# Kernel optimization log

Measured on AMD Instinct MI355X. Metric: run time of the kernel, lower is better.

## Reference

```python
import jax, jax.numpy as jnp
import numpy as np

N, E = 50000, 800000
IN, HID, H1, H2, OUT = 128, 64, 4, 6, 121
NEG_SLOPE = 0.2


def setup_inputs() -> dict:
    key = jax.random.key(0)
    ks = jax.random.split(key, 16)
    s = 0.1  # weight init scale
    return {
        "x": jax.random.normal(ks[0], (N, IN), jnp.float32),
        "src": jax.random.randint(ks[1], (E,), 0, N),
        "dst": jax.random.randint(ks[2], (E,), 0, N),
        # conv1: in=IN, heads=H1, out=HID, concat
        "W1": jax.random.normal(ks[3], (IN, H1 * HID), jnp.float32) * s,
        "a1_src": jax.random.normal(ks[4], (H1, HID), jnp.float32) * s,
        "a1_dst": jax.random.normal(ks[5], (H1, HID), jnp.float32) * s,
        "b1": jnp.zeros((H1 * HID,), jnp.float32),
        # conv2: in=H1*HID, heads=H1, out=HID, concat, residual
        "W2": jax.random.normal(ks[6], (H1 * HID, H1 * HID), jnp.float32) * s,
        "a2_src": jax.random.normal(ks[7], (H1, HID), jnp.float32) * s,
        "a2_dst": jax.random.normal(ks[8], (H1, HID), jnp.float32) * s,
        "b2": jnp.zeros((H1 * HID,), jnp.float32),
        "Wres2": jax.random.normal(ks[9], (H1 * HID, H1 * HID), jnp.float32) * s,
        # conv3: in=H1*HID, heads=H2, out=OUT, mean (concat=False)
        "W3": jax.random.normal(ks[10], (H1 * HID, H2 * OUT), jnp.float32) * s,
        "a3_src": jax.random.normal(ks[11], (H2, OUT), jnp.float32) * s,
        "a3_dst": jax.random.normal(ks[12], (H2, OUT), jnp.float32) * s,
        "b3": jnp.zeros((OUT,), jnp.float32),
    }


def _segment_softmax(e, seg, n):
    # e: [E, H], softmax over edges sharing the same destination node
    m = jax.ops.segment_max(e, seg, num_segments=n)
    ex = jnp.exp(e - m[seg])
    s = jax.ops.segment_sum(ex, seg, num_segments=n)
    return ex / (s[seg] + 1e-16)


def _gat_conv(x, src, dst, W, a_src, a_dst, b, heads, ch, concat, Wres=None):
    n = x.shape[0]
    h = (x @ W).reshape(n, heads, ch)                       # [N, H, C]
    al_s = jnp.sum(h * a_src, axis=-1)                      # [N, H]
    al_d = jnp.sum(h * a_dst, axis=-1)                      # [N, H]
    e = jax.nn.leaky_relu(al_s[src] + al_d[dst], NEG_SLOPE)  # [E, H]
    alpha = _segment_softmax(e, dst, n)                     # [E, H]
    msg = h[src] * alpha[..., None]                         # [E, H, C]
    out = jax.ops.segment_sum(msg, dst, num_segments=n)     # [N, H, C]
    out = out.reshape(n, heads * ch) if concat else out.mean(axis=1)
    if Wres is not None:
        out = out + x @ Wres
    return out + b


def reference(x, src, dst, W1, a1_src, a1_dst, b1, W2, a2_src, a2_dst, b2,
              Wres2, W3, a3_src, a3_dst, b3):
    n = x.shape[0]
    # PyG GATConv default: add self-loops
    loop = jnp.arange(n, dtype=src.dtype)
    s = jnp.concatenate([src, loop])
    d = jnp.concatenate([dst, loop])
    h = jax.nn.elu(_gat_conv(x, s, d, W1, a1_src, a1_dst, b1, H1, HID, True))
    h = jax.nn.elu(_gat_conv(h, s, d, W2, a2_src, a2_dst, b2, H1, HID, True, Wres=Wres2))
    h = _gat_conv(h, s, d, W3, a3_src, a3_dst, b3, H2, OUT, False)
    return jax.nn.sigmoid(h)
```

## Files before the change

kernel.cpp:

```cpp
#include <hip/hip_runtime.h>
#include <hip/hip_bf16.h>


#define NODES 50000
#define EDGES 800000
#define MPAD  50048
#define C0    25088
#define C1    24912

typedef unsigned short u16;
typedef __attribute__((ext_vector_type(8))) short bf16x8;
typedef __attribute__((ext_vector_type(4))) float f32x4;

__device__ __forceinline__ float bf16f(u16 r) {
    return __uint_as_float(((unsigned)r) << 16);
}
__device__ __forceinline__ u16 f2b(float v) {
    __hip_bfloat16 b = __float2bfloat16(v);
    return *(u16*)&b;
}
__device__ __forceinline__ float blo(unsigned d) { return __uint_as_float(d << 16); }
__device__ __forceinline__ float bhi(unsigned d) { return __uint_as_float(d & 0xffff0000u); }


__global__ void fill_ones_kernel(int* __restrict__ deg, int n) {
    int i = blockIdx.x * blockDim.x + threadIdx.x;
    if (i < n) deg[i] = 1;
}

__global__ void hist_kernel(const int* __restrict__ dst, int* __restrict__ deg, int E) {
    int e = blockIdx.x * blockDim.x + threadIdx.x;
    if (e < E) atomicAdd(&deg[dst[e]], 1);
}

__global__ void deg_bsum_kernel(const int* __restrict__ deg, int* __restrict__ bsum, int n) {
    int tid = threadIdx.x, lane = tid & 63, wid = tid >> 6;
    int i = blockIdx.x * 256 + tid;
    int v = (i < n) ? deg[i] : 0;
    #pragma unroll
    for (int ofs = 32; ofs > 0; ofs >>= 1) v += __shfl_down(v, ofs);
    __shared__ int sp[4];
    if (lane == 0) sp[wid] = v;
    __syncthreads();
    if (tid == 0) bsum[blockIdx.x] = sp[0] + sp[1] + sp[2] + sp[3];
}

__global__ void bsum_scan_kernel(int* __restrict__ bsum, int* __restrict__ row_ptr,
                                 int nb, int n) {
    int tid = threadIdx.x, lane = tid & 63, wid = tid >> 6;
    int v = (tid < nb) ? bsum[tid] : 0;
    int incl = v;
    #pragma unroll
    for (int ofs = 1; ofs < 64; ofs <<= 1) {
        int t = __shfl_up(incl, ofs);
        if (lane >= ofs) incl += t;
    }
    __shared__ int sp[4];
    if (lane == 63) sp[wid] = incl;
    __syncthreads();
    int add = 0;
    for (int k = 0; k < wid; k++) add += sp[k];
    int excl = incl - v + add;
    if (tid < nb) bsum[tid] = excl;
    if (tid == nb - 1) row_ptr[n] = excl + v;
}

__global__ void deg_scan_kernel(const int* __restrict__ deg, const int* __restrict__ bofs,
                                int* __restrict__ row_ptr, int* __restrict__ cursor, int n) {
    int tid = threadIdx.x, lane = tid & 63, wid = tid >> 6;
    int i = blockIdx.x * 256 + tid;
    int v = (i < n) ? deg[i] : 0;
    int incl = v;
    #pragma unroll
    for (int ofs = 1; ofs < 64; ofs <<= 1) {
        int t = __shfl_up(incl, ofs);
        if (lane >= ofs) incl += t;
    }
    __shared__ int sp[4];
    if (lane == 63) sp[wid] = incl;
    __syncthreads();
    int add = bofs[blockIdx.x];
    for (int k = 0; k < wid; k++) add += sp[k];
    int excl = incl - v + add;
    if (i < n) { row_ptr[i] = excl; cursor[i] = excl; }
}

__global__ void scatter_kernel(const int* __restrict__ src, const int* __restrict__ dst,
                               int E, int n, int* __restrict__ cursor, int* __restrict__ csr_src) {
    int e = blockIdx.x * blockDim.x + threadIdx.x;
    if (e < E) {
        int d = dst[e];
        int p = atomicAdd(&cursor[d], 1);
        csr_src[p] = src[e];
    } else if (e < E + n) {
        int i = e - E;
        int p = atomicAdd(&cursor[i], 1);
        csr_src[p] = i;
    }
}


__global__ void convertA4_kernel(const float* __restrict__ A, u16* __restrict__ O, int total4) {
    int idx = blockIdx.x * blockDim.x + threadIdx.x;
    if (idx >= total4) return;
    float4 f = ((const float4*)A)[idx];
    ushort4 o;
    o.x = f2b(f.x); o.y = f2b(f.y); o.z = f2b(f.z); o.w = f2b(f.w);
    ((ushort4*)O)[idx] = o;
}

__global__ void convertW_kernel(const float* __restrict__ W, int ldw, int col0,
                                int Ncols, int Npad, int K, u16* __restrict__ WT) {
    int idx = blockIdx.x * blockDim.x + threadIdx.x;
    if (idx >= Npad * K) return;
    int k = idx % K;
    int n = idx / K;
    float f = (n < Ncols) ? W[(size_t)k * ldw + col0 + n] : 0.f;
    WT[(size_t)n * K + k] = f2b(f);
}

__global__ void convertW3stack_kernel(const float* __restrict__ W3, u16* __restrict__ WT) {
    int idx = blockIdx.x * blockDim.x + threadIdx.x;
    if (idx >= 128 * 1536) return;
    int q = idx % 1536;
    int n = idx / 1536;
    int h = q >> 8, k = q & 255;
    float f = (n < 121) ? W3[(size_t)k * 726 + h * 121 + n] : 0.f;
    WT[(size_t)n * 1536 + q] = f2b(f);
}

__global__ void prep_cmat_kernel(const float* __restrict__ W3, const float* __restrict__ a3s,
                                 const float* __restrict__ a3d, float* __restrict__ cm) {
    int idx = blockIdx.x * blockDim.x + threadIdx.x;
    if (idx >= 12 * 256) return;
    int k = idx & 255;
    int o = idx >> 8;
    int h = (o < 6) ? o : o - 6;
    const float* a = (o < 6) ? a3s : a3d;
    float v = 0.f;
    for (int c = 0; c < 121; c++) v += W3[(size_t)k * 726 + h * 121 + c] * a[h * 121 + c];
    cm[(size_t)o * 256 + k] = v;
}


__global__ __launch_bounds__(256) void gemm_mfma_kernel(
    const u16* __restrict__ A, const u16* __restrict__ B,
    u16* __restrict__ Cb, u16* __restrict__ Cb2,
    int M, int Ncols, int K2, int ldc, int split) {
    __shared__ __align__(16) u16 As[128][40];
    __shared__ __align__(16) u16 Bs[128][40];
    int tid = threadIdx.x;
    int lane = tid & 63;
    int wv = tid >> 6;
    int quad = lane >> 4, lm = lane & 15;
    int wm = (wv & 1) * 64, wn = (wv >> 1) * 64;
    int bm = blockIdx.x * 128, bn = blockIdx.y * 128;

    f32x4 zero = {0.f, 0.f, 0.f, 0.f};
    f32x4 acc[4][4];
    #pragma unroll
    for (int i = 0; i < 4; i++)
        #pragma unroll
        for (int j = 0; j < 4; j++) acc[i][j] = zero;

    for (int k0 = 0; k0 < K2; k0 += 32) {
        #pragma unroll
        for (int it = 0; it < 2; ++it) {
            int chunk = tid + it * 256;
            int row = chunk >> 2, seg = chunk & 3;
            uint4 va = *(const uint4*)(A + (size_t)(bm + row) * K2 + k0 + seg * 8);
            uint4 vb = *(const uint4*)(B + (size_t)(bn + row) * K2 + k0 + seg * 8);
            *(uint4*)&As[row][seg * 8] = va;
            *(uint4*)&Bs[row][seg * 8] = vb;
        }
        __syncthreads();
        bf16x8 af[4], bfr[4];
        #pragma unroll
        for (int i = 0; i < 4; i++) af[i] = *(const bf16x8*)&As[wm + i * 16 + lm][quad * 8];
        #pragma unroll
        for (int j = 0; j < 4; j++) bfr[j] = *(const bf16x8*)&Bs[wn + j * 16 + lm][quad * 8];
        #pragma unroll
        for (int i = 0; i < 4; i++)
            #pragma unroll
            for (int j = 0; j < 4; j++)
                acc[i][j] = __builtin_amdgcn_mfma_f32_16x16x32_bf16(af[i], bfr[j], acc[i][j], 0, 0, 0);
        __syncthreads();
    }

    #pragma unroll
    for (int i = 0; i < 4; i++) {
        #pragma unroll
        for (int j = 0; j < 4; j++) {
            int col = bn + wn + j * 16 + lm;
            if (col >= Ncols) continue;
            int row_base = bm + wm + i * 16 + quad * 4;
            #pragma unroll
            for (int r = 0; r < 4; r++) {
                int row = row_base + r;
                if (row >= M) continue;
                float v = acc[i][j][r];
                if (col < split) Cb[(size_t)row * ldc + col] = f2b(v);
                else             Cb2[(size_t)row * ldc + col - split] = f2b(v);
            }
        }
    }
}


__global__ __launch_bounds__(256) void gemm_skinny(
    const u16* __restrict__ A, const u16* __restrict__ B,
    float* __restrict__ C, const float* __restrict__ bias, int count) {
    __shared__ __align__(16) u16 Bs[128][40];
    int tid = threadIdx.x, lane = tid & 63, wv = tid >> 6;
    int quad = lane >> 4, lm = lane & 15;
    int bm = blockIdx.x * 32;
    int mrow = (wv >> 1) * 16;
    int ncol = (wv & 1) * 64;
    int arow = bm + mrow + lm;
    if (arow >= count) arow = count - 1;
    const u16* Ap = A + (size_t)arow * 1536;

    f32x4 zero = {0.f, 0.f, 0.f, 0.f};
    f32x4 acc[4];
    #pragma unroll
    for (int j = 0; j < 4; j++) acc[j] = zero;

    for (int k0 = 0; k0 < 1536; k0 += 32) {
        #pragma unroll
        for (int it = 0; it < 2; ++it) {
            int chunk = tid + it * 256;
            int r = chunk >> 2, s = chunk & 3;
            *(uint4*)&Bs[r][s * 8] = *(const uint4*)(B + (size_t)r * 1536 + k0 + s * 8);
        }
        bf16x8 af = *(const bf16x8*)(Ap + k0 + quad * 8);
        __syncthreads();
        #pragma unroll
        for (int j = 0; j < 4; j++) {
            bf16x8 bf = *(const bf16x8*)&Bs[ncol + j * 16 + lm][quad * 8];
            acc[j] = __builtin_amdgcn_mfma_f32_16x16x32_bf16(af, bf, acc[j], 0, 0, 0);
        }
        __syncthreads();
    }

    #pragma unroll
    for (int j = 0; j < 4; j++) {
        int col = ncol + j * 16 + lm;
        if (col >= 121) continue;
        int row_base = bm + mrow + quad * 4;
        #pragma unroll
        for (int r = 0; r < 4; r++) {
            int row = row_base + r;
            if (row >= count) continue;
            float v = acc[j][r] + bias[col];
            v = 1.f / (1.f + __expf(-v));
            C[(size_t)row * 121 + col] = v;
        }
    }
}


__global__ void row_alpha4_kernel(const u16* __restrict__ f, const float* __restrict__ a_s,
                                  const float* __restrict__ a_d, float* __restrict__ al_s,
                                  float* __restrict__ al_d, int n) {
    int wv = threadIdx.x >> 6, lane = threadIdx.x & 63;
    int i = blockIdx.x * 4 + wv;
    if (i >= n) return;
    ushort4 hv = *(const ushort4*)(f + (size_t)i * 256 + lane * 4);
    float4 as = *(const float4*)(a_s + lane * 4);
    float4 ad = *(const float4*)(a_d + lane * 4);
    float x0 = bf16f(hv.x), x1 = bf16f(hv.y), x2 = bf16f(hv.z), x3 = bf16f(hv.w);
    float ps = x0 * as.x + x1 * as.y + x2 * as.z + x3 * as.w;
    float pd = x0 * ad.x + x1 * ad.y + x2 * ad.z + x3 * ad.w;
    #pragma unroll
    for (int ofs = 1; ofs < 16; ofs <<= 1) {
        ps += __shfl_xor(ps, ofs);
        pd += __shfl_xor(pd, ofs);
    }
    if ((lane & 15) == 0) {
        int hd = lane >> 4;
        al_s[(size_t)i * 4 + hd] = ps;
        al_d[(size_t)i * 4 + hd] = pd;
    }
}

__global__ __launch_bounds__(256) void al3_kernel(const u16* __restrict__ o2b,
                                                  const float* __restrict__ cm,
                                                  float* __restrict__ al3, int n) {
    int wid = threadIdx.x >> 6, lane = threadIdx.x & 63;
    int i = blockIdx.x * 4 + wid;
    if (i >= n) return;
    uint2 d = *(const uint2*)(o2b + (size_t)i * 256 + lane * 4);
    float v0 = blo(d.x), v1 = bhi(d.x), v2 = blo(d.y), v3 = bhi(d.y);
    float a[12];
    #pragma unroll
    for (int o = 0; o < 12; o++) {
        float4 c = *(const float4*)(cm + (size_t)o * 256 + lane * 4);
        a[o] = v0 * c.x + v1 * c.y + v2 * c.z + v3 * c.w;
    }
    #pragma unroll
    for (int ofs = 1; ofs < 64; ofs <<= 1) {
        #pragma unroll
        for (int o = 0; o < 12; o++) a[o] += __shfl_xor(a[o], ofs);
    }
    if (lane == 0) {
        float4* dst = (float4*)(al3 + (size_t)i * 12);
        dst[0] = make_float4(a[0], a[1], a[2], a[3]);
        dst[1] = make_float4(a[4], a[5], a[6], a[7]);
        dst[2] = make_float4(a[8], a[9], a[10], a[11]);
    }
}


__global__ __launch_bounds__(256) void agg4_fused(
    const u16* __restrict__ f, const float* __restrict__ al_s, const float* __restrict__ al_d,
    const int* __restrict__ row_ptr, const int* __restrict__ csr_src,
    const float* __restrict__ bias, const u16* __restrict__ resb,
    u16* __restrict__ outb, int n) {
    int wid = threadIdx.x >> 6, lane = threadIdx.x & 63;
    int i = blockIdx.x * 4 + wid;
    if (i >= n) return;
    int beg = row_ptr[i], end = row_ptr[i + 1];
    int h_st = lane >> 4;
    int el = lane & 15;
    int half = lane >> 5;
    int c8 = (lane & 31) * 8;
    float ald_st = al_d[(size_t)i * 4 + h_st];
    float acc[8] = {};
    float S = 0.f;
    for (int base = beg; base < end; base += 16) {
        int cnt = min(16, end - base);
        int idxv = csr_src[base + min(el, cnt - 1)];
        float av = al_s[(size_t)idxv * 4 + h_st] + ald_st;
        av = av > 0.f ? av : 0.2f * av;
        float ex = __expf(fminf(av, 60.f));
        for (int e = 0; e < cnt; e += 2) {
            int ei = e + half;
            int eu = ei < cnt ? ei : e;
            int s = __shfl(idxv, eu);
            float w = __shfl(ex, ((lane & 24) << 1) | eu);
            if (ei >= cnt) w = 0.f;
            S += w;
            uint4 d = *(const uint4*)(f + (size_t)s * 256 + c8);
            acc[0] = fmaf(w, blo(d.x), acc[0]); acc[1] = fmaf(w, bhi(d.x), acc[1]);
            acc[2] = fmaf(w, blo(d.y), acc[2]); acc[3] = fmaf(w, bhi(d.y), acc[3]);
            acc[4] = fmaf(w, blo(d.z), acc[4]); acc[5] = fmaf(w, bhi(d.z), acc[5]);
            acc[6] = fmaf(w, blo(d.w), acc[6]); acc[7] = fmaf(w, bhi(d.w), acc[7]);
        }
    }
    #pragma unroll
    for (int k = 0; k < 8; k++) acc[k] += __shfl_xor(acc[k], 32);
    S += __shfl_xor(S, 32);
    if (half == 0) {
        float inv = 1.f / (S + 1e-16f);
        float4 b0 = *(const float4*)(bias + c8);
        float4 b1 = *(const float4*)(bias + c8 + 4);
        float v[8];
        v[0] = acc[0] * inv + b0.x; v[1] = acc[1] * inv + b0.y;
        v[2] = acc[2] * inv + b0.z; v[3] = acc[3] * inv + b0.w;
        v[4] = acc[4] * inv + b1.x; v[5] = acc[5] * inv + b1.y;
        v[6] = acc[6] * inv + b1.z; v[7] = acc[7] * inv + b1.w;
        if (resb) {
            uint4 r = *(const uint4*)(resb + (size_t)i * 256 + c8);
            v[0] += blo(r.x); v[1] += bhi(r.x); v[2] += blo(r.y); v[3] += bhi(r.y);
            v[4] += blo(r.z); v[5] += bhi(r.z); v[6] += blo(r.w); v[7] += bhi(r.w);
        }
        #pragma unroll
        for (int k = 0; k < 8; k++) v[k] = v[k] > 0.f ? v[k] : (__expf(v[k]) - 1.f);
        uint4 o;
        o.x = (unsigned)f2b(v[0]) | ((unsigned)f2b(v[1]) << 16);
        o.y = (unsigned)f2b(v[2]) | ((unsigned)f2b(v[3]) << 16);
        o.z = (unsigned)f2b(v[4]) | ((unsigned)f2b(v[5]) << 16);
        o.w = (unsigned)f2b(v[6]) | ((unsigned)f2b(v[7]) << 16);
        *(uint4*)(outb + (size_t)i * 256 + c8) = o;
    }
}


__global__ __launch_bounds__(256) void aggS_fused(
    const u16* __restrict__ x, const float* __restrict__ al3,
    const int* __restrict__ row_ptr, const int* __restrict__ csr_src,
    u16* __restrict__ S, int node0, int count) {
    __shared__ int s_i[4][16];
    __shared__ float s_w[4][96];
    int wid = threadIdx.x >> 6, lane = threadIdx.x & 63;
    int li = blockIdx.x * 4 + wid;
    if (li >= count) return;
    int i = node0 + li;
    int beg = row_ptr[i], end = row_ptr[i + 1];
    int half = lane >> 5;
    int c8 = (lane & 31) * 8;
    int e16 = lane & 15;
    int hA = lane >> 4;
    int hB = 4 + (lane >> 4);
    float aldA = al3[(size_t)i * 12 + 6 + hA];
    float aldB = (lane < 32) ? al3[(size_t)i * 12 + 6 + hB] : 0.f;
    float acc[6][8] = {};
    float Ssum[6] = {};
    for (int base = beg; base < end; base += 16) {
        int cnt = min(16, end - base);
        int idxe = csr_src[base + min(e16, cnt - 1)];
        if (lane < 16) s_i[wid][lane] = idxe;
        float vA = al3[(size_t)idxe * 12 + hA] + aldA;
        vA = vA > 0.f ? vA : 0.2f * vA;
        float exA = __expf(fminf(vA, 60.f));
        if (e16 < cnt) s_w[wid][e16 * 6 + hA] = exA;
        if (lane < 32) {
            float vB = al3[(size_t)idxe * 12 + hB] + aldB;
            vB = vB > 0.f ? vB : 0.2f * vB;
            float exB = __expf(fminf(vB, 60.f));
            if (e16 < cnt) s_w[wid][e16 * 6 + hB] = exB;
        }
        for (int e = 0; e < cnt; e += 2) {
            int ei = e + half;
            bool valid = ei < cnt;
            int eu = valid ? ei : e;
            int s = s_i[wid][eu];
            uint4 d = *(const uint4*)(x + (size_t)s * 256 + c8);
            float v0 = blo(d.x), v1 = bhi(d.x), v2 = blo(d.y), v3 = bhi(d.y);
            float v4 = blo(d.z), v5 = bhi(d.z), v6 = blo(d.w), v7 = bhi(d.w);
            #pragma unroll
            for (int hh = 0; hh < 6; hh++) {
                float w = valid ? s_w[wid][eu * 6 + hh] : 0.f;
                Ssum[hh] += w;
                acc[hh][0] = fmaf(w, v0, acc[hh][0]);
                acc[hh][1] = fmaf(w, v1, acc[hh][1]);
                acc[hh][2] = fmaf(w, v2, acc[hh][2]);
                acc[hh][3] = fmaf(w, v3, acc[hh][3]);
                acc[hh][4] = fmaf(w, v4, acc[hh][4]);
                acc[hh][5] = fmaf(w, v5, acc[hh][5]);
                acc[hh][6] = fmaf(w, v6, acc[hh][6]);
                acc[hh][7] = fmaf(w, v7, acc[hh][7]);
            }
        }
    }
    #pragma unroll
    for (int hh = 0; hh < 6; hh++) {
        Ssum[hh] += __shfl_xor(Ssum[hh], 32);
        #pragma unroll
        for (int k = 0; k < 8; k++) acc[hh][k] += __shfl_xor(acc[hh][k], 32);
    }
    if (half == 0) {
        #pragma unroll
        for (int hh = 0; hh < 6; hh++) {
            float inv = 1.f / (6.f * (Ssum[hh] + 1e-16f));
            uint4 o;
            o.x = (unsigned)f2b(acc[hh][0] * inv) | ((unsigned)f2b(acc[hh][1] * inv) << 16);
            o.y = (unsigned)f2b(acc[hh][2] * inv) | ((unsigned)f2b(acc[hh][3] * inv) << 16);
            o.z = (unsigned)f2b(acc[hh][4] * inv) | ((unsigned)f2b(acc[hh][5] * inv) << 16);
            o.w = (unsigned)f2b(acc[hh][6] * inv) | ((unsigned)f2b(acc[hh][7] * inv) << 16);
            *(uint4*)(S + (size_t)li * 1536 + hh * 256 + c8) = o;
        }
    }
}


extern "C" void kernel_launch(void* const* d_in, const int* in_sizes, int n_in,
                              void* d_out, int out_size, void* d_ws, size_t ws_size,
                              hipStream_t stream) {
    const float* x      = (const float*)d_in[0];
    const int*   src    = (const int*)d_in[1];
    const int*   dst    = (const int*)d_in[2];
    const float* W1     = (const float*)d_in[3];
    const float* a1_src = (const float*)d_in[4];
    const float* a1_dst = (const float*)d_in[5];
    const float* b1     = (const float*)d_in[6];
    const float* W2     = (const float*)d_in[7];
    const float* a2_src = (const float*)d_in[8];
    const float* a2_dst = (const float*)d_in[9];
    const float* b2     = (const float*)d_in[10];
    const float* Wres2  = (const float*)d_in[11];
    const float* W3     = (const float*)d_in[12];
    const float* a3_src = (const float*)d_in[13];
    const float* a3_dst = (const float*)d_in[14];
    const float* b3     = (const float*)d_in[15];
    float* out = (float*)d_out;

    const int N = NODES, E = EDGES;
    const int EN = E + N;
    const int NB = (N + 255) / 256;

    char* p = (char*)d_ws;
    auto alloc = [&](size_t bytes) -> char* {
        char* r = p;
        p += (bytes + 511) & ~(size_t)511;
        return r;
    };
    int*   row_ptr = (int*)alloc((size_t)(N + 1) * sizeof(int));
    int*   cursor  = (int*)alloc((size_t)N * sizeof(int));
    int*   deg     = (int*)alloc((size_t)N * sizeof(int));
    int*   bsum    = (int*)alloc(256 * sizeof(int));
    int*   csr_src = (int*)alloc((size_t)EN * sizeof(int));
    float* al      = (float*)alloc((size_t)N * 12 * sizeof(float));
    float* cm      = (float*)alloc((size_t)12 * 256 * sizeof(float));
    u16*   o2b     = (u16*)alloc((size_t)MPAD * 256 * sizeof(u16));
    u16*   WT2     = (u16*)alloc((size_t)512 * 256 * sizeof(u16));
    u16*   W3sT    = (u16*)alloc((size_t)128 * 1536 * sizeof(u16));
    const size_t A2B_B  = (size_t)MPAD * 256 * sizeof(u16);
    const size_t F1B_B  = (size_t)N * 256 * sizeof(u16);
    const size_t RESB_B = (size_t)N * 256 * sizeof(u16);
    const size_t S_B    = (size_t)C0 * 1536 * sizeof(u16);
    size_t r2_bytes = A2B_B + F1B_B + RESB_B;
    if (S_B > r2_bytes) r2_bytes = S_B;
    char* r2 = alloc(r2_bytes + 1024);
    u16* A2b  = (u16*)r2;
    u16* f1b  = (u16*)(r2 + A2B_B);
    u16* resb = (u16*)(r2 + A2B_B + F1B_B);
    u16* A2a  = (u16*)(r2 + A2B_B + F1B_B);
    u16* Sb   = (u16*)r2;
    (void)ws_size; (void)n_in; (void)in_sizes; (void)out_size;

    float* al_s = al;
    float* al_d = al + (size_t)4 * N;

    fill_ones_kernel<<<NB, 256, 0, stream>>>(deg, N);
    hist_kernel<<<(E + 255) / 256, 256, 0, stream>>>(dst, deg, E);
    deg_bsum_kernel<<<NB, 256, 0, stream>>>(deg, bsum, N);
    bsum_scan_kernel<<<1, 256, 0, stream>>>(bsum, row_ptr, NB, N);
    deg_scan_kernel<<<NB, 256, 0, stream>>>(deg, bsum, row_ptr, cursor, N);
    scatter_kernel<<<(E + N + 255) / 256, 256, 0, stream>>>(src, dst, E, N, cursor, csr_src);

    int nwb = (N + 3) / 4;

    convertA4_kernel<<<(N * 128 / 4 + 255) / 256, 256, 0, stream>>>(x, A2a, N * 128 / 4);
    convertW_kernel<<<(256 * 128 + 255) / 256, 256, 0, stream>>>(W1, 256, 0, 256, 256, 128, WT2);
    {
        dim3 g(MPAD / 128, 2);
        gemm_mfma_kernel<<<g, 256, 0, stream>>>(A2a, WT2, f1b, nullptr, N, 256, 128, 256, 9999);
    }
    row_alpha4_kernel<<<nwb, 256, 0, stream>>>(f1b, a1_src, a1_dst, al_s, al_d, N);
    agg4_fused<<<nwb, 256, 0, stream>>>(f1b, al_s, al_d, row_ptr, csr_src, b1, nullptr, A2b, N);

    convertW_kernel<<<(256 * 256 + 255) / 256, 256, 0, stream>>>(W2, 256, 0, 256, 256, 256, WT2);
    convertW_kernel<<<(256 * 256 + 255) / 256, 256, 0, stream>>>(Wres2, 256, 0, 256, 256, 256,
                                                                 WT2 + (size_t)256 * 256);
    {
        dim3 g(MPAD / 128, 4);
        gemm_mfma_kernel<<<g, 256, 0, stream>>>(A2b, WT2, f1b, resb, N, 512, 256, 256, 256);
    }
    row_alpha4_kernel<<<nwb, 256, 0, stream>>>(f1b, a2_src, a2_dst, al_s, al_d, N);
    agg4_fused<<<nwb, 256, 0, stream>>>(f1b, al_s, al_d, row_ptr, csr_src, b2, resb, o2b, N);

    prep_cmat_kernel<<<(12 * 256 + 255) / 256, 256, 0, stream>>>(W3, a3_src, a3_dst, cm);
    al3_kernel<<<nwb, 256, 0, stream>>>(o2b, cm, al, N);
    convertW3stack_kernel<<<(128 * 1536 + 255) / 256, 256, 0, stream>>>(W3, W3sT);
    {
        aggS_fused<<<(C0 + 3) / 4, 256, 0, stream>>>(o2b, al, row_ptr, csr_src, Sb, 0, C0);
        gemm_skinny<<<(C0 + 31) / 32, 256, 0, stream>>>(Sb, W3sT, out, b3, C0);
        aggS_fused<<<(C1 + 3) / 4, 256, 0, stream>>>(o2b, al, row_ptr, csr_src, Sb, C0, C1);
        gemm_skinny<<<(C1 + 31) / 32, 256, 0, stream>>>(Sb, W3sT, out + (size_t)C0 * 121, b3, C1);
    }
}
```

Measured before the change: 701.5 us.

## Fold attention-logit projections into weights and fuse prep and alpha kernels

Merges all weight conversions and the attention projection vectors (W·a) into one prep kernel. Layer-1 logits are computed from x during bf16 conversion, and later-layer logits are computed inside the previous aggregation epilogue. This removes the separate row_alpha/al3 passes and re-reads of the feature matrix. The final gemm now uses 64-row tiles with shared A staging, and aggS switches to 4 channels per lane without half-warp edge splitting. These trade extra epilogue FLOPs and different numerics (logits from fp32 instead of bf16 features) for fewer launches and memory passes.

```diff
diff --git a/kernel.cpp b/kernel.cpp
--- a/kernel.cpp
+++ b/kernel.cpp
@@ -100,46 +100,77 @@
 }
 
 
-__global__ void convertA4_kernel(const float* __restrict__ A, u16* __restrict__ O, int total4) {
-    int idx = blockIdx.x * blockDim.x + threadIdx.x;
-    if (idx >= total4) return;
-    float4 f = ((const float4*)A)[idx];
-    ushort4 o;
-    o.x = f2b(f.x); o.y = f2b(f.y); o.z = f2b(f.z); o.w = f2b(f.w);
-    ((ushort4*)O)[idx] = o;
-}
-
-__global__ void convertW_kernel(const float* __restrict__ W, int ldw, int col0,
-                                int Ncols, int Npad, int K, u16* __restrict__ WT) {
-    int idx = blockIdx.x * blockDim.x + threadIdx.x;
-    if (idx >= Npad * K) return;
-    int k = idx % K;
-    int n = idx / K;
-    float f = (n < Ncols) ? W[(size_t)k * ldw + col0 + n] : 0.f;
-    WT[(size_t)n * K + k] = f2b(f);
-}
-
-__global__ void convertW3stack_kernel(const float* __restrict__ W3, u16* __restrict__ WT) {
-    int idx = blockIdx.x * blockDim.x + threadIdx.x;
-    if (idx >= 128 * 1536) return;
-    int q = idx % 1536;
-    int n = idx / 1536;
-    int h = q >> 8, k = q & 255;
-    float f = (n < 121) ? W3[(size_t)k * 726 + h * 121 + n] : 0.f;
-    WT[(size_t)n * 1536 + q] = f2b(f);
-}
-
-__global__ void prep_cmat_kernel(const float* __restrict__ W3, const float* __restrict__ a3s,
-                                 const float* __restrict__ a3d, float* __restrict__ cm) {
-    int idx = blockIdx.x * blockDim.x + threadIdx.x;
-    if (idx >= 12 * 256) return;
-    int k = idx & 255;
-    int o = idx >> 8;
-    int h = (o < 6) ? o : o - 6;
-    const float* a = (o < 6) ? a3s : a3d;
-    float v = 0.f;
-    for (int c = 0; c < 121; c++) v += W3[(size_t)k * 726 + h * 121 + c] * a[h * 121 + c];
-    cm[(size_t)o * 256 + k] = v;
+__global__ void prep_weights(
+    const float* __restrict__ W1, const float* __restrict__ W2,
+    const float* __restrict__ Wres2, const float* __restrict__ W3,
+    const float* __restrict__ a1s, const float* __restrict__ a1d,
+    const float* __restrict__ a2s, const float* __restrict__ a2d,
+    const float* __restrict__ a3s, const float* __restrict__ a3d,
+    u16* __restrict__ WT1, u16* __restrict__ WT2, u16* __restrict__ W3sT,
+    float* __restrict__ q1t, float* __restrict__ q2t, float* __restrict__ cm) {
+    int idx = blockIdx.x * 256 + threadIdx.x;
+    if (idx < 32768) {
+        int n = idx >> 7, k = idx & 127;
+        WT1[idx] = f2b(W1[(size_t)k * 256 + n]);
+    } else if ((idx -= 32768) < 131072) {
+        int n = idx >> 8, k = idx & 255;
+        float v = (n < 256) ? W2[(size_t)k * 256 + n] : Wres2[(size_t)k * 256 + (n - 256)];
+        WT2[idx] = f2b(v);
+    } else if ((idx -= 131072) < 196608) {
+        int n = idx / 1536, q = idx % 1536;
+        int h = q >> 8, k = q & 255;
+        W3sT[idx] = f2b((n < 121) ? W3[(size_t)k * 726 + h * 121 + n] : 0.f);
+    } else if ((idx -= 196608) < 1024) {
+        int h = idx >> 7, k = idx & 127;
+        int hh = h & 3;
+        const float* a = (h < 4) ? a1s : a1d;
+        float v = 0.f;
+        for (int c = 0; c < 64; c++) v += W1[(size_t)k * 256 + hh * 64 + c] * a[hh * 64 + c];
+        q1t[idx] = v;
+    } else if ((idx -= 1024) < 2048) {
+        int h = idx >> 8, k = idx & 255;
+        int hh = h & 3;
+        const float* a = (h < 4) ? a2s : a2d;
+        float v = 0.f;
+        for (int c = 0; c < 64; c++) v += W2[(size_t)k * 256 + hh * 64 + c] * a[hh * 64 + c];
+        q2t[idx] = v;
+    } else if ((idx -= 2048) < 3072) {
+        int o = idx >> 8, k = idx & 255;
+        int h = (o < 6) ? o : o - 6;
+        const float* a = (o < 6) ? a3s : a3d;
+        float v = 0.f;
+        for (int c = 0; c < 121; c++) v += W3[(size_t)k * 726 + h * 121 + c] * a[h * 121 + c];
+        cm[idx] = v;
+    }
+}
+#define PREP_TOTAL (32768 + 131072 + 196608 + 1024 + 2048 + 3072)
+
+
+__global__ __launch_bounds__(256) void convx_al1(
+    const float* __restrict__ x, const float* __restrict__ q1t,
+    u16* __restrict__ A2a, float* __restrict__ alA, int n) {
+    int wid = threadIdx.x >> 6, lane = threadIdx.x & 63;
+    int i = blockIdx.x * 4 + wid;
+    if (i >= n) return;
+    float2 xv = *(const float2*)(x + (size_t)i * 128 + lane * 2);
+    ushort2 o;
+    o.x = f2b(xv.x); o.y = f2b(xv.y);
+    *(ushort2*)(A2a + (size_t)i * 128 + lane * 2) = o;
+    float p[8];
+    #pragma unroll
+    for (int h = 0; h < 8; h++) {
+        float2 q = *(const float2*)(q1t + h * 128 + lane * 2);
+        p[h] = xv.x * q.x + xv.y * q.y;
+    }
+    #pragma unroll
+    for (int ofs = 1; ofs <= 32; ofs <<= 1) {
+        #pragma unroll
+        for (int h = 0; h < 8; h++) p[h] += __shfl_xor(p[h], ofs);
+    }
+    if (lane == 0) {
+        *(float4*)(alA + (size_t)i * 8)     = make_float4(p[0], p[1], p[2], p[3]);
+        *(float4*)(alA + (size_t)i * 8 + 4) = make_float4(p[4], p[5], p[6], p[7]);
+    }
 }
 
 
@@ -207,115 +238,75 @@
 }
 
 
-__global__ __launch_bounds__(256) void gemm_skinny(
+__global__ __launch_bounds__(256) void gemm_skinny64(
     const u16* __restrict__ A, const u16* __restrict__ B,
     float* __restrict__ C, const float* __restrict__ bias, int count) {
+    __shared__ __align__(16) u16 As[64][40];
     __shared__ __align__(16) u16 Bs[128][40];
     int tid = threadIdx.x, lane = tid & 63, wv = tid >> 6;
     int quad = lane >> 4, lm = lane & 15;
-    int bm = blockIdx.x * 32;
-    int mrow = (wv >> 1) * 16;
-    int ncol = (wv & 1) * 64;
-    int arow = bm + mrow + lm;
-    if (arow >= count) arow = count - 1;
-    const u16* Ap = A + (size_t)arow * 1536;
+    int bm = blockIdx.x * 64;
+    int mrow = (wv >> 1) * 32, ncol = (wv & 1) * 64;
+    int ar = bm + (tid >> 2);
+    if (ar >= count) ar = count - 1;
+    const u16* Ap = A + (size_t)ar * 1536 + (tid & 3) * 8;
 
     f32x4 zero = {0.f, 0.f, 0.f, 0.f};
-    f32x4 acc[4];
-    #pragma unroll
-    for (int j = 0; j < 4; j++) acc[j] = zero;
+    f32x4 acc[2][4];
+    #pragma unroll
+    for (int i = 0; i < 2; i++)
+        #pragma unroll
+        for (int j = 0; j < 4; j++) acc[i][j] = zero;
 
     for (int k0 = 0; k0 < 1536; k0 += 32) {
+        *(uint4*)&As[tid >> 2][(tid & 3) * 8] = *(const uint4*)(Ap + k0);
         #pragma unroll
         for (int it = 0; it < 2; ++it) {
-            int chunk = tid + it * 256;
-            int r = chunk >> 2, s = chunk & 3;
-            *(uint4*)&Bs[r][s * 8] = *(const uint4*)(B + (size_t)r * 1536 + k0 + s * 8);
-        }
-        bf16x8 af = *(const bf16x8*)(Ap + k0 + quad * 8);
+            int t = tid + it * 256;
+            *(uint4*)&Bs[t >> 2][(t & 3) * 8] =
+                *(const uint4*)(B + (size_t)(t >> 2) * 1536 + k0 + (t & 3) * 8);
+        }
         __syncthreads();
+        bf16x8 af[2], bfr[4];
+        #pragma unroll
+        for (int i = 0; i < 2; i++) af[i] = *(const bf16x8*)&As[mrow + i * 16 + lm][quad * 8];
+        #pragma unroll
+        for (int j = 0; j < 4; j++) bfr[j] = *(const bf16x8*)&Bs[ncol + j * 16 + lm][quad * 8];
+        #pragma unroll
+        for (int i = 0; i < 2; i++)
+            #pragma unroll
+            for (int j = 0; j < 4; j++)
+                acc[i][j] = __builtin_amdgcn_mfma_f32_16x16x32_bf16(af[i], bfr[j], acc[i][j], 0, 0, 0);
+        __syncthreads();
+    }
+
+    #pragma unroll
+    for (int i = 0; i < 2; i++) {
         #pragma unroll
         for (int j = 0; j < 4; j++) {
-            bf16x8 bf = *(const bf16x8*)&Bs[ncol + j * 16 + lm][quad * 8];
-            acc[j] = __builtin_amdgcn_mfma_f32_16x16x32_bf16(af, bf, acc[j], 0, 0, 0);
-        }
-        __syncthreads();
-    }
-
-    #pragma unroll
-    for (int j = 0; j < 4; j++) {
-        int col = ncol + j * 16 + lm;
-        if (col >= 121) continue;
-        int row_base = bm + mrow + quad * 4;
-        #pragma unroll
-        for (int r = 0; r < 4; r++) {
-            int row = row_base + r;
-            if (row >= count) continue;
-            float v = acc[j][r] + bias[col];
-            v = 1.f / (1.f + __expf(-v));
-            C[(size_t)row * 121 + col] = v;
-        }
-    }
-}
-
-
-__global__ void row_alpha4_kernel(const u16* __restrict__ f, const float* __restrict__ a_s,
-                                  const float* __restrict__ a_d, float* __restrict__ al_s,
-                                  float* __restrict__ al_d, int n) {
-    int wv = threadIdx.x >> 6, lane = threadIdx.x & 63;
-    int i = blockIdx.x * 4 + wv;
-    if (i >= n) return;
-    ushort4 hv = *(const ushort4*)(f + (size_t)i * 256 + lane * 4);
-    float4 as = *(const float4*)(a_s + lane * 4);
-    float4 ad = *(const float4*)(a_d + lane * 4);
-    float x0 = bf16f(hv.x), x1 = bf16f(hv.y), x2 = bf16f(hv.z), x3 = bf16f(hv.w);
-    float ps = x0 * as.x + x1 * as.y + x2 * as.z + x3 * as.w;
-    float pd = x0 * ad.x + x1 * ad.y + x2 * ad.z + x3 * ad.w;
-    #pragma unroll
-    for (int ofs = 1; ofs < 16; ofs <<= 1) {
-        ps += __shfl_xor(ps, ofs);
-        pd += __shfl_xor(pd, ofs);
-    }
-    if ((lane & 15) == 0) {
-        int hd = lane >> 4;
-        al_s[(size_t)i * 4 + hd] = ps;
-        al_d[(size_t)i * 4 + hd] = pd;
-    }
-}
-
-__global__ __launch_bounds__(256) void al3_kernel(const u16* __restrict__ o2b,
-                                                  const float* __restrict__ cm,
-                                                  float* __restrict__ al3, int n) {
-    int wid = threadIdx.x >> 6, lane = threadIdx.x & 63;
-    int i = blockIdx.x * 4 + wid;
-    if (i >= n) return;
-    uint2 d = *(const uint2*)(o2b + (size_t)i * 256 + lane * 4);
-    float v0 = blo(d.x), v1 = bhi(d.x), v2 = blo(d.y), v3 = bhi(d.y);
-    float a[12];
-    #pragma unroll
-    for (int o = 0; o < 12; o++) {
-        float4 c = *(const float4*)(cm + (size_t)o * 256 + lane * 4);
-        a[o] = v0 * c.x + v1 * c.y + v2 * c.z + v3 * c.w;
-    }
-    #pragma unroll
-    for (int ofs = 1; ofs < 64; ofs <<= 1) {
-        #pragma unroll
-        for (int o = 0; o < 12; o++) a[o] += __shfl_xor(a[o], ofs);
-    }
-    if (lane == 0) {
-        float4* dst = (float4*)(al3 + (size_t)i * 12);
-        dst[0] = make_float4(a[0], a[1], a[2], a[3]);
-        dst[1] = make_float4(a[4], a[5], a[6], a[7]);
-        dst[2] = make_float4(a[8], a[9], a[10], a[11]);
+            int col = ncol + j * 16 + lm;
+            if (col >= 121) continue;
+            int row_base = bm + mrow + i * 16 + quad * 4;
+            #pragma unroll
+            for (int r = 0; r < 4; r++) {
+                int row = row_base + r;
+                if (row >= count) continue;
+                float v = acc[i][j][r] + bias[col];
+                v = 1.f / (1.f + __expf(-v));
+                C[(size_t)row * 121 + col] = v;
+            }
+        }
     }
 }
 
 
 __global__ __launch_bounds__(256) void agg4_fused(
-    const u16* __restrict__ f, const float* __restrict__ al_s, const float* __restrict__ al_d,
+    const u16* __restrict__ f, const float* __restrict__ al8,
     const int* __restrict__ row_ptr, const int* __restrict__ csr_src,
     const float* __restrict__ bias, const u16* __restrict__ resb,
-    u16* __restrict__ outb, int n) {
+    u16* __restrict__ outb,
+    const float* __restrict__ q8, float* __restrict__ alB,
+    const float* __restrict__ q12, float* __restrict__ al12, int n) {
     int wid = threadIdx.x >> 6, lane = threadIdx.x & 63;
     int i = blockIdx.x * 4 + wid;
     if (i >= n) return;
@@ -324,13 +315,13 @@
     int el = lane & 15;
     int half = lane >> 5;
     int c8 = (lane & 31) * 8;
-    float ald_st = al_d[(size_t)i * 4 + h_st];
+    float ald_st = al8[(size_t)i * 8 + 4 + h_st];
     float acc[8] = {};
     float S = 0.f;
     for (int base = beg; base < end; base += 16) {
         int cnt = min(16, end - base);
         int idxv = csr_src[base + min(el, cnt - 1)];
-        float av = al_s[(size_t)idxv * 4 + h_st] + ald_st;
+        float av = al8[(size_t)idxv * 8 + h_st] + ald_st;
         av = av > 0.f ? av : 0.2f * av;
         float ex = __expf(fminf(av, 60.f));
         for (int e = 0; e < cnt; e += 2) {
@@ -372,6 +363,47 @@
         o.z = (unsigned)f2b(v[4]) | ((unsigned)f2b(v[5]) << 16);
         o.w = (unsigned)f2b(v[6]) | ((unsigned)f2b(v[7]) << 16);
         *(uint4*)(outb + (size_t)i * 256 + c8) = o;
+        if (alB) {
+            float pj[8];
+            #pragma unroll
+            for (int h = 0; h < 8; h++) {
+                const float* qp = q8 + h * 256 + c8;
+                float4 qa = *(const float4*)qp;
+                float4 qb = *(const float4*)(qp + 4);
+                pj[h] = v[0] * qa.x + v[1] * qa.y + v[2] * qa.z + v[3] * qa.w
+                      + v[4] * qb.x + v[5] * qb.y + v[6] * qb.z + v[7] * qb.w;
+            }
+            #pragma unroll
+            for (int ofs = 1; ofs <= 16; ofs <<= 1) {
+                #pragma unroll
+                for (int h = 0; h < 8; h++) pj[h] += __shfl_xor(pj[h], ofs);
+            }
+            if (lane == 0) {
+                *(float4*)(alB + (size_t)i * 8)     = make_float4(pj[0], pj[1], pj[2], pj[3]);
+                *(float4*)(alB + (size_t)i * 8 + 4) = make_float4(pj[4], pj[5], pj[6], pj[7]);
+            }
+        }
+        if (al12) {
+            float pj[12];
+            #pragma unroll
+            for (int o12 = 0; o12 < 12; o12++) {
+                const float* qp = q12 + o12 * 256 + c8;
+                float4 qa = *(const float4*)qp;
+                float4 qb = *(const float4*)(qp + 4);
+                pj[o12] = v[0] * qa.x + v[1] * qa.y + v[2] * qa.z + v[3] * qa.w
+                        + v[4] * qb.x + v[5] * qb.y + v[6] * qb.z + v[7] * qb.w;
+            }
+            #pragma unroll
+            for (int ofs = 1; ofs <= 16; ofs <<= 1) {
+                #pragma unroll
+                for (int o12 = 0; o12 < 12; o12++) pj[o12] += __shfl_xor(pj[o12], ofs);
+            }
+            if (lane == 0) {
+                *(float4*)(al12 + (size_t)i * 12)     = make_float4(pj[0], pj[1], pj[2], pj[3]);
+                *(float4*)(al12 + (size_t)i * 12 + 4) = make_float4(pj[4], pj[5], pj[6], pj[7]);
+                *(float4*)(al12 + (size_t)i * 12 + 8) = make_float4(pj[8], pj[9], pj[10], pj[11]);
+            }
+        }
     }
 }
 
@@ -387,14 +419,13 @@
     if (li >= count) return;
     int i = node0 + li;
     int beg = row_ptr[i], end = row_ptr[i + 1];
-    int half = lane >> 5;
-    int c8 = (lane & 31) * 8;
+    int c4 = lane * 4;
     int e16 = lane & 15;
     int hA = lane >> 4;
     int hB = 4 + (lane >> 4);
     float aldA = al3[(size_t)i * 12 + 6 + hA];
     float aldB = (lane < 32) ? al3[(size_t)i * 12 + 6 + hB] : 0.f;
-    float acc[6][8] = {};
+    float acc[6][4] = {};
     float Ssum[6] = {};
     for (int base = beg; base < end; base += 16) {
         int cnt = min(16, end - base);
@@ -410,46 +441,30 @@
             float exB = __expf(fminf(vB, 60.f));
             if (e16 < cnt) s_w[wid][e16 * 6 + hB] = exB;
         }
-        for (int e = 0; e < cnt; e += 2) {
-            int ei = e + half;
-            bool valid = ei < cnt;
-            int eu = valid ? ei : e;
-            int s = s_i[wid][eu];
-            uint4 d = *(const uint4*)(x + (size_t)s * 256 + c8);
+        for (int e = 0; e < cnt; e++) {
+            int s = s_i[wid][e];
+            uint2 d = *(const uint2*)(x + (size_t)s * 256 + c4);
             float v0 = blo(d.x), v1 = bhi(d.x), v2 = blo(d.y), v3 = bhi(d.y);
-            float v4 = blo(d.z), v5 = bhi(d.z), v6 = blo(d.w), v7 = bhi(d.w);
             #pragma unroll
             for (int hh = 0; hh < 6; hh++) {
-                float w = valid ? s_w[wid][eu * 6 + hh] : 0.f;
+                float w = s_w[wid][e * 6 + hh];
                 Ssum[hh] += w;
                 acc[hh][0] = fmaf(w, v0, acc[hh][0]);
                 acc[hh][1] = fmaf(w, v1, acc[hh][1]);
                 acc[hh][2] = fmaf(w, v2, acc[hh][2]);
                 acc[hh][3] = fmaf(w, v3, acc[hh][3]);
-                acc[hh][4] = fmaf(w, v4, acc[hh][4]);
-                acc[hh][5] = fmaf(w, v5, acc[hh][5]);
-                acc[hh][6] = fmaf(w, v6, acc[hh][6]);
-                acc[hh][7] = fmaf(w, v7, acc[hh][7]);
             }
         }
     }
     #pragma unroll
     for (int hh = 0; hh < 6; hh++) {
-        Ssum[hh] += __shfl_xor(Ssum[hh], 32);
-        #pragma unroll
-        for (int k = 0; k < 8; k++) acc[hh][k] += __shfl_xor(acc[hh][k], 32);
-    }
-    if (half == 0) {
-        #pragma unroll
-        for (int hh = 0; hh < 6; hh++) {
-            float inv = 1.f / (6.f * (Ssum[hh] + 1e-16f));
-            uint4 o;
-            o.x = (unsigned)f2b(acc[hh][0] * inv) | ((unsigned)f2b(acc[hh][1] * inv) << 16);
-            o.y = (unsigned)f2b(acc[hh][2] * inv) | ((unsigned)f2b(acc[hh][3] * inv) << 16);
-            o.z = (unsigned)f2b(acc[hh][4] * inv) | ((unsigned)f2b(acc[hh][5] * inv) << 16);
-            o.w = (unsigned)f2b(acc[hh][6] * inv) | ((unsigned)f2b(acc[hh][7] * inv) << 16);
-            *(uint4*)(S + (size_t)li * 1536 + hh * 256 + c8) = o;
-        }
+        float inv = 1.f / (6.f * (Ssum[hh] + 1e-16f));
+        ushort4 o;
+        o.x = f2b(acc[hh][0] * inv);
+        o.y = f2b(acc[hh][1] * inv);
+        o.z = f2b(acc[hh][2] * inv);
+        o.w = f2b(acc[hh][3] * inv);
+        *(ushort4*)(S + (size_t)li * 1536 + hh * 256 + c4) = o;
     }
 }
 
@@ -490,11 +505,16 @@
     int*   deg     = (int*)alloc((size_t)N * sizeof(int));
     int*   bsum    = (int*)alloc(256 * sizeof(int));
     int*   csr_src = (int*)alloc((size_t)EN * sizeof(int));
-    float* al      = (float*)alloc((size_t)N * 12 * sizeof(float));
+    float* alA     = (float*)alloc((size_t)N * 8 * sizeof(float));
+    float* alB     = (float*)alloc((size_t)N * 8 * sizeof(float));
+    float* al3     = (float*)alloc((size_t)N * 12 * sizeof(float));
+    float* q1t     = (float*)alloc((size_t)8 * 128 * sizeof(float));
+    float* q2t     = (float*)alloc((size_t)8 * 256 * sizeof(float));
     float* cm      = (float*)alloc((size_t)12 * 256 * sizeof(float));
-    u16*   o2b     = (u16*)alloc((size_t)MPAD * 256 * sizeof(u16));
+    u16*   WT1     = (u16*)alloc((size_t)256 * 128 * sizeof(u16));
     u16*   WT2     = (u16*)alloc((size_t)512 * 256 * sizeof(u16));
     u16*   W3sT    = (u16*)alloc((size_t)128 * 1536 * sizeof(u16));
+    u16*   o2b     = (u16*)alloc((size_t)MPAD * 256 * sizeof(u16));
     const size_t A2B_B  = (size_t)MPAD * 256 * sizeof(u16);
     const size_t F1B_B  = (size_t)N * 256 * sizeof(u16);
     const size_t RESB_B = (size_t)N * 256 * sizeof(u16);
@@ -509,9 +529,6 @@
     u16* Sb   = (u16*)r2;
     (void)ws_size; (void)n_in; (void)in_sizes; (void)out_size;
 
-    float* al_s = al;
-    float* al_d = al + (size_t)4 * N;
-
     fill_ones_kernel<<<NB, 256, 0, stream>>>(deg, N);
     hist_kernel<<<(E + 255) / 256, 256, 0, stream>>>(dst, deg, E);
     deg_bsum_kernel<<<NB, 256, 0, stream>>>(deg, bsum, N);
@@ -521,32 +538,29 @@
 
     int nwb = (N + 3) / 4;
 
-    convertA4_kernel<<<(N * 128 / 4 + 255) / 256, 256, 0, stream>>>(x, A2a, N * 128 / 4);
-    convertW_kernel<<<(256 * 128 + 255) / 256, 256, 0, stream>>>(W1, 256, 0, 256, 256, 128, WT2);
+    prep_weights<<<(PREP_TOTAL + 255) / 256, 256, 0, stream>>>(
+        W1, W2, Wres2, W3, a1_src, a1_dst, a2_src, a2_dst, a3_src, a3_dst,
+        WT1, WT2, W3sT, q1t, q2t, cm);
+
+    convx_al1<<<nwb, 256, 0, stream>>>(x, q1t, A2a, alA, N);
     {
         dim3 g(MPAD / 128, 2);
-        gemm_mfma_kernel<<<g, 256, 0, stream>>>(A2a, WT2, f1b, nullptr, N, 256, 128, 256, 9999);
-    }
-    row_alpha4_kernel<<<nwb, 256, 0, stream>>>(f1b, a1_src, a1_dst, al_s, al_d, N);
-    agg4_fused<<<nwb, 256, 0, stream>>>(f1b, al_s, al_d, row_ptr, csr_src, b1, nullptr, A2b, N);
-
-    convertW_kernel<<<(256 * 256 + 255) / 256, 256, 0, stream>>>(W2, 256, 0, 256, 256, 256, WT2);
-    convertW_kernel<<<(256 * 256 + 255) / 256, 256, 0, stream>>>(Wres2, 256, 0, 256, 256, 256,
-                                                                 WT2 + (size_t)256 * 256);
+        gemm_mfma_kernel<<<g, 256, 0, stream>>>(A2a, WT1, f1b, nullptr, N, 256, 128, 256, 9999);
+    }
+    agg4_fused<<<nwb, 256, 0, stream>>>(f1b, alA, row_ptr, csr_src, b1, nullptr, A2b,
+                                        q2t, alB, nullptr, nullptr, N);
+
     {
         dim3 g(MPAD / 128, 4);
         gemm_mfma_kernel<<<g, 256, 0, stream>>>(A2b, WT2, f1b, resb, N, 512, 256, 256, 256);
     }
-    row_alpha4_kernel<<<nwb, 256, 0, stream>>>(f1b, a2_src, a2_dst, al_s, al_d, N);
-    agg4_fused<<<nwb, 256, 0, stream>>>(f1b, al_s, al_d, row_ptr, csr_src, b2, resb, o2b, N);
-
-    prep_cmat_kernel<<<(12 * 256 + 255) / 256, 256, 0, stream>>>(W3, a3_src, a3_dst, cm);
-    al3_kernel<<<nwb, 256, 0, stream>>>(o2b, cm, al, N);
-    convertW3stack_kernel<<<(128 * 1536 + 255) / 256, 256, 0, stream>>>(W3, W3sT);
+    agg4_fused<<<nwb, 256, 0, stream>>>(f1b, alB, row_ptr, csr_src, b2, resb, o2b,
+                                        nullptr, nullptr, cm, al3, N);
+
     {
-        aggS_fused<<<(C0 + 3) / 4, 256, 0, stream>>>(o2b, al, row_ptr, csr_src, Sb, 0, C0);
-        gemm_skinny<<<(C0 + 31) / 32, 256, 0, stream>>>(Sb, W3sT, out, b3, C0);
-        aggS_fused<<<(C1 + 3) / 4, 256, 0, stream>>>(o2b, al, row_ptr, csr_src, Sb, C0, C1);
-        gemm_skinny<<<(C1 + 31) / 32, 256, 0, stream>>>(Sb, W3sT, out + (size_t)C0 * 121, b3, C1);
-    }
-}
+        aggS_fused<<<(C0 + 3) / 4, 256, 0, stream>>>(o2b, al3, row_ptr, csr_src, Sb, 0, C0);
+        gemm_skinny64<<<(C0 + 63) / 64, 256, 0, stream>>>(Sb, W3sT, out, b3, C0);
+        aggS_fused<<<(C1 + 3) / 4, 256, 0, stream>>>(o2b, al3, row_ptr, csr_src, Sb, C0, C1);
+        gemm_skinny64<<<(C1 + 63) / 64, 256, 0, stream>>>(Sb, W3sT, out + (size_t)C0 * 121, b3, C1);
+    }
+}
```

After: 693.2 us. No clear change (-1.2%).
